# Optimization experiments

Measured on AMD Instinct MI355X. Metric: run time of the kernel, lower is better.

## Reference

```python
import jax, jax.numpy as jnp
import numpy as np

B, D, L = 8, 512, 8192


def log_g(x):
    # th.where(x >= 0, log(relu(x) + 1), x)
    return jnp.where(x >= 0, jnp.log1p(jnp.maximum(x, 0.0)), x)


def min_gru(hg):
    # hg: [B, H, L] -> [B, H/2, L]
    h, gate = jnp.split(hg, 2, axis=1)
    log_coeffs = -jax.nn.softplus(gate)                      # log a_t
    log_values = -jax.nn.softplus(-gate) + log_g(h)          # log b_t
    a_star = jnp.cumsum(log_coeffs, axis=2)
    log_h0_plus_b_star = jax.lax.cumlogsumexp(log_values - a_star, axis=2)
    return jnp.exp(a_star + log_h0_plus_b_star)


def conv1x1(x, w, b):
    # x: [B, D, L], w: [E, D], b: [E]  (kernel-size-1 Conv1d == pointwise linear)
    return jnp.einsum('ed,bdl->bel', w, x) + b[None, :, None]


def setup_inputs() -> dict:
    key = jax.random.key(0)
    k1, k2, k3, k4, k5 = jax.random.split(key, 5)
    scale = 1.0 / np.sqrt(D)
    x = jax.random.normal(k1, (B, D, L), dtype=jnp.float32)
    w_fore = jax.random.normal(k2, (D, D), dtype=jnp.float32) * scale
    b_fore = jax.random.normal(k3, (D,), dtype=jnp.float32) * scale
    w_back = jax.random.normal(k4, (D, D), dtype=jnp.float32) * scale
    b_back = jax.random.normal(k5, (D,), dtype=jnp.float32) * scale
    return {'x': x, 'w_fore': w_fore, 'b_fore': b_fore, 'w_back': w_back, 'b_back': b_back}


def reference(x, w_fore, b_fore, w_back, b_back):
    fore = min_gru(conv1x1(x, w_fore, b_fore))                            # [B, D/2, L]
    back = jnp.flip(min_gru(conv1x1(jnp.flip(x, 2), w_back, b_back)), 2)  # [B, D/2, L]
    return jnp.concatenate([fore, back], axis=1)                          # [B, D, L]
```

## Files before the change

kernel.cpp:

```cpp
#include <hip/hip_runtime.h>

#define BATCH 8
#define DIN   512
#define SEQ   8192
#define ECH   1024
#define HCH   256
#define CL    32
#define NCHNK (SEQ / CL)
#define NSC   16

typedef __bf16 bf16;
typedef __bf16 bf16x8 __attribute__((ext_vector_type(8)));
typedef float  floatx4 __attribute__((ext_vector_type(4)));

__device__ __forceinline__ void async_ld16(void* lds, const void* g) {
  __builtin_amdgcn_global_load_lds(
      (const __attribute__((address_space(1))) unsigned int*)g,
      (__attribute__((address_space(3))) unsigned int*)lds, 16, 0, 0);
}

__device__ __forceinline__ float bits2f(unsigned u) {
  return __builtin_bit_cast(float, u);
}

__device__ __forceinline__ void gru_ab(unsigned v, float& a, float& bt) {
  float hh = bits2f(v << 16);
  float g  = bits2f(v & 0xffff0000u);
  float eg = __expf(-g);
  float sg = 1.f / (1.f + eg);
  a = eg * sg;
  float gv = hh >= 0.f ? 1.f + hh : __expf(hh);
  bt = sg * gv;
}

__global__ void k_wconv(const float* __restrict__ wf, const float* __restrict__ bfo,
                        const float* __restrict__ wb, const float* __restrict__ bb,
                        bf16* __restrict__ Wb, float* __restrict__ bias) {
  int idx = blockIdx.x * 256 + threadIdx.x;
  if (idx < ECH * DIN) {
    int n = idx >> 9, d = idx & 511;
    int dir = n >> 9, r = n & 511, e = r >> 1, isg = r & 1;
    int s = e + (isg ? HCH : 0);
    const float* w = dir ? wb : wf;
    Wb[idx] = (bf16)w[s * DIN + d];
  }
  if (idx < ECH) {
    int dir = idx >> 9, r = idx & 511, e = r >> 1, isg = r & 1;
    int s = e + (isg ? HCH : 0);
    bias[idx] = (dir ? bb : bfo)[s];
  }
}

__global__ void k_xpose(const float* __restrict__ x, bf16* __restrict__ xT) {
  __shared__ float T[64 * 65];
  int t = threadIdx.x;
  int l0 = blockIdx.x * 64;
  int d0 = blockIdx.y * 64;
  int b  = blockIdx.z;
  const float* xb = x + (size_t)b * DIN * SEQ;
#pragma unroll
  for (int p = 0; p < 4; ++p) {
    int dl = (t >> 4) + p * 16;
    int l4 = (t & 15) * 4;
    float4 v = *(const float4*)(xb + (size_t)(d0 + dl) * SEQ + l0 + l4);
    T[dl * 65 + l4 + 0] = v.x;
    T[dl * 65 + l4 + 1] = v.y;
    T[dl * 65 + l4 + 2] = v.z;
    T[dl * 65 + l4 + 3] = v.w;
  }
  __syncthreads();
  bf16* xTb = xT + (size_t)b * SEQ * DIN;
#pragma unroll
  for (int p = 0; p < 2; ++p) {
    int ll = (t >> 3) + p * 32;
    int d8 = (t & 7) * 8;
    bf16x8 h;
#pragma unroll
    for (int j = 0; j < 8; ++j) h[j] = (bf16)T[(d8 + j) * 65 + ll];
    *(bf16x8*)(xTb + (size_t)(l0 + ll) * DIN + d0 + d8) = h;
  }
}

#define BKK 32
#define NKT (DIN / BKK)
#define CS_STRIDE 268

__launch_bounds__(512, 2)
__global__ void k_gemm(const bf16* __restrict__ xT, const bf16* __restrict__ Wb,
                       const float* __restrict__ bias, bf16* __restrict__ hg,
                       float* __restrict__ Asum, float* __restrict__ Bsum) {
  __shared__ __align__(16) bf16 lds[68608];

  int t = threadIdx.x;
  int lane = t & 63, wave = t >> 6;
  int l15 = lane & 15, quad = lane >> 4;
  int wm = wave >> 2, wn = wave & 3;

  int lin = blockIdx.x + 4 * blockIdx.y;
  int swz = (lin & 7) * 16 + (lin >> 3);
  int ntile = swz & 3, ltile = swz >> 2;
  int n0 = ntile * 256;
  int l0 = ltile * 256;
  int b  = blockIdx.z;

  const bf16* gA = xT + ((size_t)b * SEQ + l0) * DIN;
  const bf16* gB = Wb + (size_t)n0 * DIN;

  int srow = t >> 2;
  int scol = (t & 3) * 8;

  float bb4[4];
#pragma unroll
  for (int ni = 0; ni < 4; ++ni) bb4[ni] = bias[n0 + wn * 64 + ni * 16 + l15];

#define STAGE(KT) do {                                                     \
    bf16* dst = lds + ((KT) & 3) * 16384 + t * 8;                          \
    const bf16* sA = gA + (size_t)srow * DIN + (KT) * BKK + scol;          \
    const bf16* sB = gB + (size_t)srow * DIN + (KT) * BKK + scol;          \
    async_ld16(dst,         sA);                                           \
    async_ld16(dst + 4096,  sA + (size_t)128 * DIN);                       \
    async_ld16(dst + 8192,  sB);                                           \
    async_ld16(dst + 12288, sB + (size_t)128 * DIN);                       \
  } while (0)

  STAGE(0); STAGE(1); STAGE(2);

  floatx4 acc[8][4];
#pragma unroll
  for (int i = 0; i < 8; ++i)
#pragma unroll
    for (int j = 0; j < 4; ++j) acc[i][j] = (floatx4){0.f, 0.f, 0.f, 0.f};

#pragma unroll
  for (int kt = 0; kt < NKT; ++kt) {
    if (kt <= NKT - 3)      asm volatile("s_waitcnt vmcnt(8)" ::: "memory");
    else if (kt == NKT - 2) asm volatile("s_waitcnt vmcnt(4)" ::: "memory");
    else                    asm volatile("s_waitcnt vmcnt(0)" ::: "memory");
    __builtin_amdgcn_s_barrier();
    asm volatile("" ::: "memory");

    if (kt + 3 < NKT) STAGE(kt + 3);

    const bf16* As = lds + (kt & 3) * 16384;
    const bf16* Bs = As + 8192;
    bf16x8 af[8], bfr[4];
#pragma unroll
    for (int i = 0; i < 8; ++i)
      af[i] = *(const bf16x8*)(As + (wm * 128 + i * 16 + l15) * BKK + quad * 8);
#pragma unroll
    for (int i = 0; i < 4; ++i)
      bfr[i] = *(const bf16x8*)(Bs + (wn * 64 + i * 16 + l15) * BKK + quad * 8);

    __builtin_amdgcn_s_setprio(1);
#pragma unroll
    for (int mi = 0; mi < 8; ++mi)
#pragma unroll
      for (int ni = 0; ni < 4; ++ni)
        acc[mi][ni] = __builtin_amdgcn_mfma_f32_16x16x32_bf16(
            af[mi], bfr[ni], acc[mi][ni], 0, 0, 0);
    __builtin_amdgcn_s_setprio(0);
  }
#undef STAGE

  __syncthreads();

  bf16* Cs = lds;
#pragma unroll
  for (int mi = 0; mi < 8; ++mi)
#pragma unroll
    for (int ni = 0; ni < 4; ++ni)
#pragma unroll
      for (int r = 0; r < 4; ++r) {
        int row = wm * 128 + mi * 16 + quad * 4 + r;
        int col = wn * 64 + ni * 16 + l15;
        Cs[row * CS_STRIDE + col] = (bf16)(acc[mi][ni][r] + bb4[ni]);
      }
  __syncthreads();

  bf16* hgb = hg + ((size_t)b * SEQ + l0) * ECH + n0;
#pragma unroll
  for (int p = 0; p < 16; ++p) {
    int row = p * 16 + (t >> 5);
    int seg = t & 31;
    *(bf16x8*)(hgb + (size_t)row * ECH + seg * 8) =
        *(const bf16x8*)(Cs + row * CS_STRIDE + seg * 8);
  }

  int dirn = ntile >> 1;
#pragma unroll
  for (int j = 0; j < 2; ++j) {
    int u = t + j * 512;
    int c = u >> 7;
    int e = u & 127;
    float A = 1.f, Bc = 0.f;
#pragma unroll 8
    for (int i = 0; i < CL; ++i) {
      int row = c * CL + (dirn ? (CL - 1 - i) : i);
      unsigned v = *(const unsigned*)(Cs + row * CS_STRIDE + 2 * e);
      float a, bt;
      gru_ab(v, a, bt);
      A *= a;
      Bc = a * Bc + bt;
    }
    int chunkg = ltile * 8 + c;
    int eg = (ntile & 1) * 128 + e;
    size_t o = ((size_t)(b * 2 + dirn) * NCHNK + chunkg) * 256 + eg;
    Asum[o] = A;
    Bsum[o] = Bc;
  }
}

__global__ void k_scan2a(const float* __restrict__ Asum, const float* __restrict__ Bsum,
                         float* __restrict__ SA, float* __restrict__ SB) {
  int e = threadIdx.x, sc = blockIdx.x, row2 = blockIdx.y, dir = row2 & 1;
  size_t base = (size_t)row2 * NCHNK;
  float Acc = 1.f, Bcc = 0.f;
#pragma unroll
  for (int i = 0; i < 16; ++i) {
    int c = sc * 16 + (dir ? 15 - i : i);
    size_t o = (base + c) * 256 + e;
    float a = Asum[o], bv = Bsum[o];
    Acc = a * Acc;
    Bcc = a * Bcc + bv;
  }
  size_t so = ((size_t)row2 * NSC + sc) * 256 + e;
  SA[so] = Acc;
  SB[so] = Bcc;
}

__global__ void k_scan2b(const float* __restrict__ SA, const float* __restrict__ SB,
                         float* __restrict__ hsc) {
  int e = threadIdx.x, row2 = blockIdx.x, dir = row2 & 1;
  float h = 0.f;
  for (int i = 0; i < NSC; ++i) {
    int sc = dir ? NSC - 1 - i : i;
    size_t o = ((size_t)row2 * NSC + sc) * 256 + e;
    hsc[o] = h;
    h = SA[o] * h + SB[o];
  }
}

__global__ void k_scan2c(const float* __restrict__ Asum, const float* __restrict__ Bsum,
                         const float* __restrict__ hsc, float* __restrict__ hin) {
  int e = threadIdx.x, sc = blockIdx.x, row2 = blockIdx.y, dir = row2 & 1;
  float h = hsc[((size_t)row2 * NSC + sc) * 256 + e];
#pragma unroll
  for (int i = 0; i < 16; ++i) {
    int c = sc * 16 + (dir ? 15 - i : i);
    size_t o = ((size_t)row2 * NCHNK + c) * 256 + e;
    hin[o] = h;
    h = Asum[o] * h + Bsum[o];
  }
}

__global__ void k_scan3(const bf16* __restrict__ hg, const float* __restrict__ hin,
                        float* __restrict__ out) {
  __shared__ float T[256 * 33];
  int t = threadIdx.x;
  int chunk = blockIdx.x, dir = blockIdx.y, b = blockIdx.z;
  const bf16* hb = hg + (size_t)b * SEQ * ECH + dir * 512 + 2 * t;
  float h = hin[((size_t)(b * 2 + dir) * NCHNK + chunk) * 256 + t];
  int lbase = chunk * CL;
#pragma unroll 8
  for (int i = 0; i < CL; ++i) {
    int ll = dir ? (CL - 1 - i) : i;
    unsigned v = *(const unsigned*)(hb + (size_t)(lbase + ll) * ECH);
    float a, bt;
    gru_ab(v, a, bt);
    h = a * h + bt;
    T[t * 33 + ll] = h;
  }
  __syncthreads();
  float* ob = out + ((size_t)b * 512 + dir * 256) * SEQ + lbase;
#pragma unroll
  for (int p = 0; p < 8; ++p) {
    int row = p * 32 + (t >> 3);
    int c4 = (t & 7) * 4;
    float4 v4;
    v4.x = T[row * 33 + c4 + 0];
    v4.y = T[row * 33 + c4 + 1];
    v4.z = T[row * 33 + c4 + 2];
    v4.w = T[row * 33 + c4 + 3];
    *(float4*)(ob + (size_t)row * SEQ + c4) = v4;
  }
}

extern "C" void kernel_launch(void* const* d_in, const int* in_sizes, int n_in,
                              void* d_out, int out_size, void* d_ws, size_t ws_size,
                              hipStream_t stream) {
  const float* x   = (const float*)d_in[0];
  const float* wf  = (const float*)d_in[1];
  const float* bfo = (const float*)d_in[2];
  const float* wb  = (const float*)d_in[3];
  const float* bb  = (const float*)d_in[4];
  float* out = (float*)d_out;
  char* ws = (char*)d_ws;

  bf16*  xT   = (bf16*)(ws);
  bf16*  hg   = (bf16*)(ws + 67108864);
  bf16*  Wbm  = (bf16*)(ws + 201326592);
  float* bias = (float*)(ws + 202375168);
  float* Asum = (float*)(ws + 202379264);
  float* Bsum = (float*)(ws + 206573568);
  float* hin  = (float*)(ws + 210767872);
  float* SA   = (float*)(ws + 214962176);
  float* SB   = (float*)(ws + 215224320);
  float* hsc  = (float*)(ws + 215486464);

  k_wconv<<<2048, 256, 0, stream>>>(wf, bfo, wb, bb, Wbm, bias);
  k_xpose<<<dim3(SEQ / 64, DIN / 64, BATCH), 256, 0, stream>>>(x, xT);
  k_gemm<<<dim3(ECH / 256, SEQ / 256, BATCH), 512, 0, stream>>>(xT, Wbm, bias, hg,
                                                                Asum, Bsum);
  k_scan2a<<<dim3(NSC, 16), 256, 0, stream>>>(Asum, Bsum, SA, SB);
  k_scan2b<<<16, 256, 0, stream>>>(SA, SB, hsc);
  k_scan2c<<<dim3(NSC, 16), 256, 0, stream>>>(Asum, Bsum, hsc, hin);
  k_scan3<<<dim3(NCHNK, 2, BATCH), 256, 0, stream>>>(hg, hin, out);
}
```

Baseline: 390.2 us.

## Restructure GEMM mainloop into double-buffered BK=64 with swizzled LDS and phased MFMA

Raises the GEMM K-tile from 32 to 64, moves from a 4-stage ring to 2 double-buffered stages, and XOR-swizzles LDS rows to avoid bank conflicts on the wider tile. Each K-step is split into four MFMA phases separated by barriers, with the async global-to-LDS loads for upcoming tiles interleaved between phases. The aim is to cut barrier and wait overhead per K and overlap loads with compute. In exchange it adds more barriers per iteration and relies on tricky buffer-reuse ordering that could race.

```diff
diff --git a/kernel.cpp b/kernel.cpp
--- a/kernel.cpp
+++ b/kernel.cpp
@@ -81,7 +81,7 @@
   }
 }
 
-#define BKK 32
+#define BKK 64
 #define NKT (DIN / BKK)
 #define CS_STRIDE 268
 
@@ -93,7 +93,7 @@
 
   int t = threadIdx.x;
   int lane = t & 63, wave = t >> 6;
-  int l15 = lane & 15, quad = lane >> 4;
+  int l15 = lane & 15, quad = lane >> 4, swr = l15 & 7;
   int wm = wave >> 2, wn = wave & 3;
 
   int lin = blockIdx.x + 4 * blockIdx.y;
@@ -106,24 +106,27 @@
   const bf16* gA = xT + ((size_t)b * SEQ + l0) * DIN;
   const bf16* gB = Wb + (size_t)n0 * DIN;
 
-  int srow = t >> 2;
-  int scol = (t & 3) * 8;
-
   float bb4[4];
 #pragma unroll
   for (int ni = 0; ni < 4; ++ni) bb4[ni] = bias[n0 + wn * 64 + ni * 16 + l15];
 
-#define STAGE(KT) do {                                                     \
-    bf16* dst = lds + ((KT) & 3) * 16384 + t * 8;                          \
-    const bf16* sA = gA + (size_t)srow * DIN + (KT) * BKK + scol;          \
-    const bf16* sB = gB + (size_t)srow * DIN + (KT) * BKK + scol;          \
-    async_ld16(dst,         sA);                                           \
-    async_ld16(dst + 4096,  sA + (size_t)128 * DIN);                       \
-    async_ld16(dst + 8192,  sB);                                           \
-    async_ld16(dst + 12288, sB + (size_t)128 * DIN);                       \
+#define STAGE_HALF(DST, GSRC, K0) do {                                        \
+    _Pragma("unroll")                                                         \
+    for (int j = 0; j < 2; ++j) {                                             \
+      int i_ = t + j * 512;                                                   \
+      int row_ = i_ >> 3, c8_ = i_ & 7;                                       \
+      async_ld16((DST) + i_ * 8,                                              \
+                 (GSRC) + (size_t)row_ * DIN + (K0) + ((c8_ ^ (row_ & 7)) * 8)); \
+    }                                                                         \
   } while (0)
 
-  STAGE(0); STAGE(1); STAGE(2);
+  STAGE_HALF(lds +     0, gA, 0);
+  STAGE_HALF(lds +  8192, gA + (size_t)128 * DIN, 0);
+  STAGE_HALF(lds + 16384, gB, 0);
+  STAGE_HALF(lds + 24576, gB + (size_t)128 * DIN, 0);
+  STAGE_HALF(lds + 32768 + 16384, gB, BKK);
+  STAGE_HALF(lds + 32768 +     0, gA, BKK);
+  STAGE_HALF(lds + 32768 +  8192, gA + (size_t)128 * DIN, BKK);
 
   floatx4 acc[8][4];
 #pragma unroll
@@ -131,36 +134,114 @@
 #pragma unroll
     for (int j = 0; j < 4; ++j) acc[i][j] = (floatx4){0.f, 0.f, 0.f, 0.f};
 
+  asm volatile("s_waitcnt vmcnt(6)" ::: "memory");
+  __builtin_amdgcn_s_barrier();
+  asm volatile("" ::: "memory");
+
 #pragma unroll
   for (int kt = 0; kt < NKT; ++kt) {
-    if (kt <= NKT - 3)      asm volatile("s_waitcnt vmcnt(8)" ::: "memory");
-    else if (kt == NKT - 2) asm volatile("s_waitcnt vmcnt(4)" ::: "memory");
-    else                    asm volatile("s_waitcnt vmcnt(0)" ::: "memory");
+    const bf16* Ab = lds + (kt & 1) * 32768 + wm * 8192;
+    const bf16* Bb = lds + (kt & 1) * 32768 + 16384 + (wn >> 1) * 8192;
+    bf16* curb = lds + (kt & 1) * 32768;
+    bf16* nxtb = lds + ((kt & 1) ^ 1) * 32768;
+    int bro = (wn & 1) * 64 + l15;
+
+    bf16x8 af[4][2], b01[2][2], b23[2][2];
+
+#pragma unroll
+    for (int mi = 0; mi < 4; ++mi)
+#pragma unroll
+      for (int k2 = 0; k2 < 2; ++k2)
+        af[mi][k2] = *(const bf16x8*)(Ab + (mi * 16 + l15) * 64 +
+                                      (((k2 * 4 + quad) ^ swr) * 8));
+#pragma unroll
+    for (int ni = 0; ni < 2; ++ni)
+#pragma unroll
+      for (int k2 = 0; k2 < 2; ++k2)
+        b01[ni][k2] = *(const bf16x8*)(Bb + (bro + ni * 16) * 64 +
+                                       (((k2 * 4 + quad) ^ swr) * 8));
+    if (kt + 1 < NKT)
+      STAGE_HALF(nxtb + 24576, gB + (size_t)128 * DIN, (kt + 1) * BKK);
+    __builtin_amdgcn_s_barrier();
+    asm volatile("s_waitcnt lgkmcnt(0)" ::: "memory");
+    __builtin_amdgcn_s_setprio(1);
+#pragma unroll
+    for (int mi = 0; mi < 4; ++mi)
+#pragma unroll
+      for (int ni = 0; ni < 2; ++ni)
+#pragma unroll
+        for (int k2 = 0; k2 < 2; ++k2)
+          acc[mi][ni] = __builtin_amdgcn_mfma_f32_16x16x32_bf16(
+              af[mi][k2], b01[ni][k2], acc[mi][ni], 0, 0, 0);
+    __builtin_amdgcn_s_setprio(0);
     __builtin_amdgcn_s_barrier();
     asm volatile("" ::: "memory");
 
-    if (kt + 3 < NKT) STAGE(kt + 3);
-
-    const bf16* As = lds + (kt & 3) * 16384;
-    const bf16* Bs = As + 8192;
-    bf16x8 af[8], bfr[4];
-#pragma unroll
-    for (int i = 0; i < 8; ++i)
-      af[i] = *(const bf16x8*)(As + (wm * 128 + i * 16 + l15) * BKK + quad * 8);
-#pragma unroll
-    for (int i = 0; i < 4; ++i)
-      bfr[i] = *(const bf16x8*)(Bs + (wn * 64 + i * 16 + l15) * BKK + quad * 8);
-
+#pragma unroll
+    for (int ni = 0; ni < 2; ++ni)
+#pragma unroll
+      for (int k2 = 0; k2 < 2; ++k2)
+        b23[ni][k2] = *(const bf16x8*)(Bb + (bro + 32 + ni * 16) * 64 +
+                                       (((k2 * 4 + quad) ^ swr) * 8));
+    __builtin_amdgcn_s_barrier();
+    asm volatile("s_waitcnt lgkmcnt(0)" ::: "memory");
     __builtin_amdgcn_s_setprio(1);
 #pragma unroll
-    for (int mi = 0; mi < 8; ++mi)
-#pragma unroll
-      for (int ni = 0; ni < 4; ++ni)
-        acc[mi][ni] = __builtin_amdgcn_mfma_f32_16x16x32_bf16(
-            af[mi], bfr[ni], acc[mi][ni], 0, 0, 0);
+    for (int mi = 0; mi < 4; ++mi)
+#pragma unroll
+      for (int ni = 0; ni < 2; ++ni)
+#pragma unroll
+        for (int k2 = 0; k2 < 2; ++k2)
+          acc[mi][2 + ni] = __builtin_amdgcn_mfma_f32_16x16x32_bf16(
+              af[mi][k2], b23[ni][k2], acc[mi][2 + ni], 0, 0, 0);
     __builtin_amdgcn_s_setprio(0);
-  }
-#undef STAGE
+    __builtin_amdgcn_s_barrier();
+    asm volatile("" ::: "memory");
+
+#pragma unroll
+    for (int mi = 0; mi < 4; ++mi)
+#pragma unroll
+      for (int k2 = 0; k2 < 2; ++k2)
+        af[mi][k2] = *(const bf16x8*)(Ab + (64 + mi * 16 + l15) * 64 +
+                                      (((k2 * 4 + quad) ^ swr) * 8));
+    if (kt + 2 < NKT)
+      STAGE_HALF(curb + 16384, gB, (kt + 2) * BKK);
+    __builtin_amdgcn_s_barrier();
+    asm volatile("s_waitcnt lgkmcnt(0)" ::: "memory");
+    __builtin_amdgcn_s_setprio(1);
+#pragma unroll
+    for (int mi = 0; mi < 4; ++mi)
+#pragma unroll
+      for (int ni = 0; ni < 2; ++ni)
+#pragma unroll
+        for (int k2 = 0; k2 < 2; ++k2)
+          acc[4 + mi][2 + ni] = __builtin_amdgcn_mfma_f32_16x16x32_bf16(
+              af[mi][k2], b23[ni][k2], acc[4 + mi][2 + ni], 0, 0, 0);
+    __builtin_amdgcn_s_setprio(0);
+    __builtin_amdgcn_s_barrier();
+    asm volatile("" ::: "memory");
+
+    if (kt + 2 < NKT) {
+      STAGE_HALF(curb, gA, (kt + 2) * BKK);
+      STAGE_HALF(curb + 8192, gA + (size_t)128 * DIN, (kt + 2) * BKK);
+    }
+    __builtin_amdgcn_s_barrier();
+    __builtin_amdgcn_s_setprio(1);
+#pragma unroll
+    for (int mi = 0; mi < 4; ++mi)
+#pragma unroll
+      for (int ni = 0; ni < 2; ++ni)
+#pragma unroll
+        for (int k2 = 0; k2 < 2; ++k2)
+          acc[4 + mi][ni] = __builtin_amdgcn_mfma_f32_16x16x32_bf16(
+              af[mi][k2], b01[ni][k2], acc[4 + mi][ni], 0, 0, 0);
+    __builtin_amdgcn_s_setprio(0);
+    if (kt <= NKT - 3)      asm volatile("s_waitcnt vmcnt(6)" ::: "memory");
+    else if (kt == NKT - 2) asm volatile("s_waitcnt vmcnt(0)" ::: "memory");
+    __builtin_amdgcn_s_barrier();
+    asm volatile("" ::: "memory");
+  }
+#undef STAGE_HALF
 
   __syncthreads();
 
```

Result: no change. 390.0 us (-0.0%).
